# Kernel optimization log

Hardware: AMD Instinct MI355X
Metric: run time of the kernel (lower is better)

The kernel has to match this reference:

```python
import jax, jax.numpy as jnp
import numpy as np

CP_SIZE = 2
CP_RANK = 0
SLIDING_WINDOW = 1024
S_GLOBAL = 4096
T_LOCAL = S_GLOBAL // CP_SIZE
NQ, NK, HN = 16, 8, 128


def setup_inputs() -> dict:
    key = jax.random.key(0)
    kq, kk, kv = jax.random.split(key, 3)
    return {
        # local zigzag-sliced queries on this cp rank: [t_local, nq, hn]
        "query": jax.random.normal(kq, (T_LOCAL, NQ, HN), dtype=jnp.float32),
        # K/V AFTER all-gather across cp ranks (rank-chunk concatenated layout,
        # exactly what gather_from_sequence_parallel_region produces): [S, nk, hn]
        "key": jax.random.normal(kk, (S_GLOBAL, NK, HN), dtype=jnp.float32),
        "value": jax.random.normal(kv, (S_GLOBAL, NK, HN), dtype=jnp.float32),
        # global packed-seq boundaries (single sub-sequence)
        "cu_seqlens": jnp.array([0, S_GLOBAL], dtype=jnp.int32),
    }


def _zigzag_perm(seq_len_global: int, cp: int) -> jnp.ndarray:
    """global position g -> offset into the rank-gathered K/V tensor."""
    cs = seq_len_global // (2 * cp)
    g = jnp.arange(seq_len_global)
    q_idx = g // cs
    owner = jnp.where(q_idx < cp, q_idx, 2 * cp - 1 - q_idx)
    local_in_rank = jnp.where(q_idx < cp, g - owner * cs,
                              cs + (g - (2 * cp - 1 - owner) * cs))
    return owner * (2 * cs) + local_in_rank


def _zigzag_rows(local_len: int, rank: int, cp: int) -> jnp.ndarray:
    """global positions of this rank's local Q tokens (zigzag layout)."""
    cs = local_len // 2
    first = jnp.arange(rank * cs, (rank + 1) * cs)
    second = jnp.arange((2 * cp - rank - 1) * cs, (2 * cp - rank) * cs)
    return jnp.concatenate([first, second])


def reference(query, key, value, cu_seqlens):
    S = key.shape[0]
    t_local, nq, hn = query.shape
    nk = key.shape[1]
    scale = hn ** (-0.5)

    # un-permute gathered K/V from rank-chunk zigzag layout to global order
    perm = _zigzag_perm(S, CP_SIZE)
    k_full = key[perm]    # [S, nk, hn]
    v_full = value[perm]

    # GQA: replicate kv heads to match q heads (enable_gqa)
    rep = nq // nk
    k_full = jnp.repeat(k_full, rep, axis=1)  # [S, nq, hn]
    v_full = jnp.repeat(v_full, rep, axis=1)

    # causal + sliding-window mask from zigzag global row indices
    row = _zigzag_rows(t_local, CP_RANK, CP_SIZE)  # [t_local]
    col = jnp.arange(S)
    forbid = col[None, :] > row[:, None]
    if SLIDING_WINDOW is not None and SLIDING_WINDOW > 0:
        forbid = forbid | (col[None, :] < row[:, None] - (SLIDING_WINDOW - 1))
    bias = jnp.where(forbid, jnp.finfo(query.dtype).min, 0.0).astype(query.dtype)

    # SDPA: scores [nq, t_local, S]
    scores = jnp.einsum('shd,thd->hst', query, k_full) * scale + bias[None]
    probs = jax.nn.softmax(scores, axis=-1)
    out = jnp.einsum('hst,thd->shd', probs, v_full)  # [t_local, nq, hn]
    return out.reshape(t_local, nq * hn)
```

## Files before the change

### kernel.cpp

```cpp
#include <hip/hip_runtime.h>
#include <hip/hip_bf16.h>

#define T_LOCAL 2048
#define S_GLOBAL 4096
#define NQ 16
#define NK 8
#define HN 128

#define SCALE2 0.12753102541996022f

typedef __attribute__((ext_vector_type(8))) short short8;
typedef __attribute__((ext_vector_type(4))) float f32x4;

static __device__ __forceinline__ ushort f2bf(float x) {
  unsigned u = __builtin_bit_cast(unsigned, x);
  unsigned r = (u + 0x7fffu + ((u >> 16) & 1u)) >> 16;
  return (ushort)r;
}

static __device__ __forceinline__ void gload16(const ushort* g, ushort* lds) {
  __builtin_amdgcn_global_load_lds(
      (const __attribute__((address_space(1))) void*)g,
      (__attribute__((address_space(3))) void*)lds, 16, 0, 0);
}

__global__ void k_convert(const float* __restrict__ K, ushort* __restrict__ Kb) {
  size_t i = ((size_t)blockIdx.x * 256 + threadIdx.x) * 4;
  float4 v = *(const float4*)(K + i);
  ushort4 o;
  o.x = f2bf(v.x); o.y = f2bf(v.y); o.z = f2bf(v.z); o.w = f2bf(v.w);
  *(ushort4*)(Kb + i) = o;
}

__global__ void v_transpose(const float* __restrict__ V, ushort* __restrict__ Vt) {
  int bid = blockIdx.x;
  int h  = bid >> 7;
  int r  = bid & 127;
  int d0 = (r >> 6) << 6;
  int p0 = (r & 63) << 6;
  __shared__ ushort tile[64][72];
  int tx = threadIdx.x & 15, ty = threadIdx.x >> 4;
  #pragma unroll
  for (int it = 0; it < 4; ++it) {
    int p = p0 + it * 16 + ty;
    int d = tx * 4;
    float4 v = *(const float4*)(V + ((size_t)p * NK + h) * HN + d0 + d);
    tile[d + 0][it * 16 + ty] = f2bf(v.x);
    tile[d + 1][it * 16 + ty] = f2bf(v.y);
    tile[d + 2][it * 16 + ty] = f2bf(v.z);
    tile[d + 3][it * 16 + ty] = f2bf(v.w);
  }
  __syncthreads();
  #pragma unroll
  for (int it = 0; it < 4; ++it) {
    int d  = it * 16 + ty;
    int pb = tx * 4;
    ushort4 o;
    o.x = tile[d][pb + 0]; o.y = tile[d][pb + 1];
    o.z = tile[d][pb + 2]; o.w = tile[d][pb + 3];
    *(ushort4*)(Vt + ((size_t)h * HN + d0 + d) * S_GLOBAL + p0 + pb) = o;
  }
}

__global__ __launch_bounds__(512, 4)
void attn_kernel(const float* __restrict__ Q, const ushort* __restrict__ Kb,
                 const ushort* __restrict__ Vt, float* __restrict__ Out) {
  __shared__ ushort Klds[2][64 * 128];
  __shared__ ushort Vlds[2][128 * 64];
  __shared__ ushort Pl[8][16][56];

  const int lane = threadIdx.x & 63;
  const int w    = threadIdx.x >> 6;
  const int qg   = w & 3;
  const int ks   = w >> 2;
  const int qcol = lane & 15;
  const int g    = lane >> 4;

  const int bid  = blockIdx.x;
  const int kvh  = bid & 7;
  const int j    = bid >> 3;
  const int head = 2 * kvh + (j & 1);
  const int slot = j >> 1;
  const int Tt   = (slot & 1) ? 16 + (slot >> 1) : (slot >> 1);
  const int tb   = Tt << 6;
  const int tw   = tb + qg * 16;
  const int tq   = tw + qcol;

  int c0, nC, a0 = 0, n;
  if (tb < 1024) { c0 = 0; nC = Tt + 1; n = nC; }
  else { c0 = 16; nC = Tt - 15; a0 = Tt + 32; n = nC + (32 - Tt); }

  short8 qf[4];
  {
    const float* qb = Q + ((size_t)tq * NQ + head) * HN;
    #pragma unroll
    for (int ds = 0; ds < 4; ++ds) {
      const float4* p4 = (const float4*)(qb + ds * 32 + g * 8);
      float4 a = p4[0], b = p4[1];
      short8 f;
      f[0] = f2bf(a.x); f[1] = f2bf(a.y); f[2] = f2bf(a.z); f[3] = f2bf(a.w);
      f[4] = f2bf(b.x); f[5] = f2bf(b.y); f[6] = f2bf(b.z); f[7] = f2bf(b.w);
      qf[ds] = f;
    }
  }
  asm volatile("s_waitcnt vmcnt(0)" ::: "memory");

  f32x4 acc[8];
  #pragma unroll
  for (int i = 0; i < 8; ++i) acc[i] = (f32x4){0.f, 0.f, 0.f, 0.f};
  float m_run = -1e30f, l_run = 0.f;

  ushort* prow = &Pl[w][qcol][0];
  const int rx = (qcol & 7) << 4;

  auto chunk_p0 = [&](int i) {
    return ((i < nC) ? (c0 + i) : (a0 + (i - nC))) << 6;
  };

  auto stage = [&](int b, int p0) {
    #pragma unroll
    for (int t = 0; t < 2; ++t) {
      int idx = (w * 2 + t) * 64 + lane;
      int row = idx >> 4;
      int cu  = (idx & 15) ^ (row & 7);
      gload16(Kb + ((size_t)(p0 + row) * NK + kvh) * HN + cu * 8,
              &Klds[b][(w * 2 + t) * 512]);
    }
    #pragma unroll
    for (int t = 0; t < 2; ++t) {
      int idx = (w * 2 + t) * 64 + lane;
      int d   = idx >> 3;
      int pu  = (idx & 7) ^ (d & 7);
      gload16(Vt + ((size_t)kvh * HN + d) * S_GLOBAL + p0 + pu * 8,
              &Vlds[b][(w * 2 + t) * 512]);
    }
  };

  stage(0, chunk_p0(0));

  for (int c = 0; c < n; ++c) {
    if (c + 1 < n) {
      stage((c + 1) & 1, chunk_p0(c + 1));
      asm volatile("s_waitcnt vmcnt(4)" ::: "memory");
    } else {
      asm volatile("s_waitcnt vmcnt(0)" ::: "memory");
    }
    __builtin_amdgcn_s_barrier();

    const int p0   = chunk_p0(c);
    const bool anti = p0 >= 2048;
    const char* Klc = (const char*)Klds[c & 1];
    const char* Vlc = (const char*)Vlds[c & 1];

    const int p0s = p0 + ks * 32;
    const bool activ = anti ? (p0s + 31 >= tw + 2049) : (p0s <= tw + 15);
    if (activ) {
      const bool needmask = anti ? (p0s < tw + 2064) : (p0s + 31 > tw);

      short8 kf[2][4];
      #pragma unroll
      for (int sub = 0; sub < 2; ++sub) {
        const int rbase = (ks * 32 + sub * 16 + qcol) * 256;
        #pragma unroll
        for (int ds = 0; ds < 4; ++ds)
          kf[sub][ds] = *(const short8*)(Klc + rbase + ((ds * 64 + g * 16) ^ rx));
      }
      short8 vf[8];
      #pragma unroll
      for (int db = 0; db < 8; ++db)
        vf[db] = *(const short8*)(Vlc + (db * 16 + qcol) * 128 + ((ks * 64 + g * 16) ^ rx));

      f32x4 st[2];
      st[0] = (f32x4){0.f, 0.f, 0.f, 0.f};
      st[1] = (f32x4){0.f, 0.f, 0.f, 0.f};
      #pragma unroll
      for (int sub = 0; sub < 2; ++sub)
        #pragma unroll
        for (int ds = 0; ds < 4; ++ds)
          st[sub] = __builtin_amdgcn_mfma_f32_16x16x32_bf16(kf[sub][ds], qf[ds], st[sub], 0, 0, 0);

      float s_[8];
      #pragma unroll
      for (int sub = 0; sub < 2; ++sub) {
        #pragma unroll
        for (int r = 0; r < 4; ++r) {
          float sv = st[sub][r] * SCALE2;
          if (needmask) {
            int p = p0s + sub * 16 + g * 4 + r;
            bool ok = anti ? (p >= tq + 2049) : (p <= tq);
            sv = ok ? sv : -INFINITY;
          }
          s_[sub * 4 + r] = sv;
        }
      }

      float mt = s_[0];
      #pragma unroll
      for (int i = 1; i < 8; ++i) mt = fmaxf(mt, s_[i]);
      mt = fmaxf(mt, __shfl_xor(mt, 16));
      mt = fmaxf(mt, __shfl_xor(mt, 32));
      float mnew = fmaxf(m_run, mt);
      float fsc  = __builtin_amdgcn_exp2f(m_run - mnew);
      float pv[8];
      float ps = 0.f;
      #pragma unroll
      for (int i = 0; i < 8; ++i) { pv[i] = __builtin_amdgcn_exp2f(s_[i] - mnew); ps += pv[i]; }
      ps += __shfl_xor(ps, 16);
      ps += __shfl_xor(ps, 32);
      l_run = l_run * fsc + ps;
      m_run = mnew;
      #pragma unroll
      for (int i = 0; i < 8; ++i) acc[i] *= fsc;

      unsigned lo0 = (unsigned)f2bf(pv[0]) | ((unsigned)f2bf(pv[1]) << 16);
      unsigned hi0 = (unsigned)f2bf(pv[2]) | ((unsigned)f2bf(pv[3]) << 16);
      unsigned lo1 = (unsigned)f2bf(pv[4]) | ((unsigned)f2bf(pv[5]) << 16);
      unsigned hi1 = (unsigned)f2bf(pv[6]) | ((unsigned)f2bf(pv[7]) << 16);
      *(uint2*)(prow + g * 4)      = make_uint2(lo0, hi0);
      *(uint2*)(prow + 16 + g * 4) = make_uint2(lo1, hi1);
      short8 pf = *(const short8*)(prow + g * 8);

      #pragma unroll
      for (int db = 0; db < 8; ++db)
        acc[db] = __builtin_amdgcn_mfma_f32_16x16x32_bf16(vf[db], pf, acc[db], 0, 0, 0);
    }
    __builtin_amdgcn_s_barrier();
  }

  __syncthreads();
  float* mb  = (float*)&Klds[0][0];
  float* mlb = (float*)&Vlds[0][0];
  if (ks == 1) {
    if (g == 0) {
      mlb[(qg * 16 + qcol) * 2 + 0] = m_run;
      mlb[(qg * 16 + qcol) * 2 + 1] = l_run;
    }
    #pragma unroll
    for (int db = 0; db < 8; ++db)
      *(f32x4*)&mb[(qg * 16 + qcol) * 128 + db * 16 + g * 4] = acc[db];
  }
  __syncthreads();
  if (ks == 0) {
    float mr = mlb[(qg * 16 + qcol) * 2 + 0];
    float lr = mlb[(qg * 16 + qcol) * 2 + 1];
    float mnew = fmaxf(m_run, mr);
    float f0 = __builtin_amdgcn_exp2f(m_run - mnew);
    float fr = __builtin_amdgcn_exp2f(mr - mnew);
    float inv = 1.0f / (l_run * f0 + lr * fr);
    float* ob = Out + (size_t)tq * (NQ * HN) + head * HN + g * 4;
    #pragma unroll
    for (int db = 0; db < 8; ++db) {
      f32x4 o = *(const f32x4*)&mb[(qg * 16 + qcol) * 128 + db * 16 + g * 4];
      float4 r;
      r.x = (acc[db][0] * f0 + o[0] * fr) * inv;
      r.y = (acc[db][1] * f0 + o[1] * fr) * inv;
      r.z = (acc[db][2] * f0 + o[2] * fr) * inv;
      r.w = (acc[db][3] * f0 + o[3] * fr) * inv;
      *(float4*)(ob + db * 16) = r;
    }
  }
}

extern "C" void kernel_launch(void* const* d_in, const int* in_sizes, int n_in,
                              void* d_out, int out_size, void* d_ws, size_t ws_size,
                              hipStream_t stream) {
  const float* Q = (const float*)d_in[0];
  const float* K = (const float*)d_in[1];
  const float* V = (const float*)d_in[2];
  float* Out = (float*)d_out;

  ushort* Kb = (ushort*)d_ws;
  ushort* Vt = Kb + (size_t)S_GLOBAL * NK * HN;

  k_convert<<<dim3((S_GLOBAL * NK * HN) / (256 * 4)), dim3(256), 0, stream>>>(K, Kb);
  v_transpose<<<dim3(NK * 2 * (S_GLOBAL / 64)), dim3(256), 0, stream>>>(V, Vt);
  attn_kernel<<<dim3(512), dim3(512), 0, stream>>>(Q, Kb, Vt, Out);
}
```

Before: 140.2 us.

## Halve block query tile, drop LDS double buffer and P round-trip via permuted K rows

Each block now handles 32 query rows with 256 threads instead of 64 rows with 512, doubling the grid to 1024 blocks and halving LDS use per block so more blocks can be resident. The K/V double buffer is removed in favour of a single buffer that is loaded and waited on synchronously every chunk. K rows are read in a permuted order so the score MFMA output layout already matches the B-operand layout needed for the PV MFMA, which removes the P write/read through LDS. The cost is that load latency is no longer overlapped within a block, and each K/V chunk is fetched by twice as many blocks.

After: 166.6 us. +18.8%, slower.

```diff
diff --git a/kernel.cpp b/kernel.cpp
--- a/kernel.cpp
+++ b/kernel.cpp
@@ -62,17 +62,16 @@
   }
 }
 
-__global__ __launch_bounds__(512, 4)
+__global__ __launch_bounds__(256, 4)
 void attn_kernel(const float* __restrict__ Q, const ushort* __restrict__ Kb,
                  const ushort* __restrict__ Vt, float* __restrict__ Out) {
-  __shared__ ushort Klds[2][64 * 128];
-  __shared__ ushort Vlds[2][128 * 64];
-  __shared__ ushort Pl[8][16][56];
+  __shared__ ushort Klds[64 * 128];
+  __shared__ ushort Vlds[128 * 64];
 
   const int lane = threadIdx.x & 63;
   const int w    = threadIdx.x >> 6;
-  const int qg   = w & 3;
-  const int ks   = w >> 2;
+  const int qg   = w & 1;
+  const int ks   = w >> 1;
   const int qcol = lane & 15;
   const int g    = lane >> 4;
 
@@ -81,14 +80,17 @@
   const int j    = bid >> 3;
   const int head = 2 * kvh + (j & 1);
   const int slot = j >> 1;
-  const int Tt   = (slot & 1) ? 16 + (slot >> 1) : (slot >> 1);
-  const int tb   = Tt << 6;
+  const int Tt   = (slot & 1) ? 32 + (slot >> 1) : (slot >> 1);
+  const int tb   = Tt << 5;
   const int tw   = tb + qg * 16;
   const int tq   = tw + qcol;
 
   int c0, nC, a0 = 0, n;
-  if (tb < 1024) { c0 = 0; nC = Tt + 1; n = nC; }
-  else { c0 = 16; nC = Tt - 15; a0 = Tt + 32; n = nC + (32 - Tt); }
+  if (tb < 1024) { c0 = 0; nC = (tb >> 6) + 1; n = nC; }
+  else {
+    c0 = 16; nC = ((tb + 31) >> 6) - 15;
+    a0 = (tb + 2049) >> 6; n = nC + (64 - a0);
+  }
 
   short8 qf[4];
   {
@@ -103,54 +105,46 @@
       qf[ds] = f;
     }
   }
-  asm volatile("s_waitcnt vmcnt(0)" ::: "memory");
 
   f32x4 acc[8];
   #pragma unroll
   for (int i = 0; i < 8; ++i) acc[i] = (f32x4){0.f, 0.f, 0.f, 0.f};
   float m_run = -1e30f, l_run = 0.f;
 
-  ushort* prow = &Pl[w][qcol][0];
-  const int rx = (qcol & 7) << 4;
+  const int rxv = (qcol & 7) << 4;
 
   auto chunk_p0 = [&](int i) {
     return ((i < nC) ? (c0 + i) : (a0 + (i - nC))) << 6;
   };
 
-  auto stage = [&](int b, int p0) {
-    #pragma unroll
-    for (int t = 0; t < 2; ++t) {
-      int idx = (w * 2 + t) * 64 + lane;
+  auto stage = [&](int p0) {
+    #pragma unroll
+    for (int t = 0; t < 4; ++t) {
+      int idx = (w * 4 + t) * 64 + lane;
       int row = idx >> 4;
       int cu  = (idx & 15) ^ (row & 7);
       gload16(Kb + ((size_t)(p0 + row) * NK + kvh) * HN + cu * 8,
-              &Klds[b][(w * 2 + t) * 512]);
-    }
-    #pragma unroll
-    for (int t = 0; t < 2; ++t) {
-      int idx = (w * 2 + t) * 64 + lane;
+              &Klds[(w * 4 + t) * 512]);
+    }
+    #pragma unroll
+    for (int t = 0; t < 4; ++t) {
+      int idx = (w * 4 + t) * 64 + lane;
       int d   = idx >> 3;
       int pu  = (idx & 7) ^ (d & 7);
       gload16(Vt + ((size_t)kvh * HN + d) * S_GLOBAL + p0 + pu * 8,
-              &Vlds[b][(w * 2 + t) * 512]);
+              &Vlds[(w * 4 + t) * 512]);
     }
   };
 
-  stage(0, chunk_p0(0));
-
   for (int c = 0; c < n; ++c) {
-    if (c + 1 < n) {
-      stage((c + 1) & 1, chunk_p0(c + 1));
-      asm volatile("s_waitcnt vmcnt(4)" ::: "memory");
-    } else {
-      asm volatile("s_waitcnt vmcnt(0)" ::: "memory");
-    }
-    __builtin_amdgcn_s_barrier();
+    stage(chunk_p0(c));
+    asm volatile("s_waitcnt vmcnt(0)" ::: "memory");
+    __syncthreads();
 
     const int p0   = chunk_p0(c);
     const bool anti = p0 >= 2048;
-    const char* Klc = (const char*)Klds[c & 1];
-    const char* Vlc = (const char*)Vlds[c & 1];
+    const char* Klc = (const char*)Klds;
+    const char* Vlc = (const char*)Vlds;
 
     const int p0s = p0 + ks * 32;
     const bool activ = anti ? (p0s + 31 >= tw + 2049) : (p0s <= tw + 15);
@@ -160,15 +154,17 @@
       short8 kf[2][4];
       #pragma unroll
       for (int sub = 0; sub < 2; ++sub) {
-        const int rbase = (ks * 32 + sub * 16 + qcol) * 256;
+        const int krow = ks * 32 + ((qcol >> 2) << 3) + sub * 4 + (qcol & 3);
+        const int rbase = krow * 256;
+        const int rxk = (krow & 7) << 4;
         #pragma unroll
         for (int ds = 0; ds < 4; ++ds)
-          kf[sub][ds] = *(const short8*)(Klc + rbase + ((ds * 64 + g * 16) ^ rx));
+          kf[sub][ds] = *(const short8*)(Klc + rbase + ((ds * 64 + g * 16) ^ rxk));
       }
       short8 vf[8];
       #pragma unroll
       for (int db = 0; db < 8; ++db)
-        vf[db] = *(const short8*)(Vlc + (db * 16 + qcol) * 128 + ((ks * 64 + g * 16) ^ rx));
+        vf[db] = *(const short8*)(Vlc + (db * 16 + qcol) * 128 + ((ks * 64 + g * 16) ^ rxv));
 
       f32x4 st[2];
       st[0] = (f32x4){0.f, 0.f, 0.f, 0.f};
@@ -186,7 +182,7 @@
         for (int r = 0; r < 4; ++r) {
           float sv = st[sub][r] * SCALE2;
           if (needmask) {
-            int p = p0s + sub * 16 + g * 4 + r;
+            int p = p0s + g * 8 + sub * 4 + r;
             bool ok = anti ? (p >= tq + 2049) : (p <= tq);
             sv = ok ? sv : -INFINITY;
           }
@@ -212,24 +208,22 @@
       #pragma unroll
       for (int i = 0; i < 8; ++i) acc[i] *= fsc;
 
-      unsigned lo0 = (unsigned)f2bf(pv[0]) | ((unsigned)f2bf(pv[1]) << 16);
-      unsigned hi0 = (unsigned)f2bf(pv[2]) | ((unsigned)f2bf(pv[3]) << 16);
-      unsigned lo1 = (unsigned)f2bf(pv[4]) | ((unsigned)f2bf(pv[5]) << 16);
-      unsigned hi1 = (unsigned)f2bf(pv[6]) | ((unsigned)f2bf(pv[7]) << 16);
-      *(uint2*)(prow + g * 4)      = make_uint2(lo0, hi0);
-      *(uint2*)(prow + 16 + g * 4) = make_uint2(lo1, hi1);
-      short8 pf = *(const short8*)(prow + g * 8);
+      uint4 pu;
+      pu.x = (unsigned)f2bf(pv[0]) | ((unsigned)f2bf(pv[1]) << 16);
+      pu.y = (unsigned)f2bf(pv[2]) | ((unsigned)f2bf(pv[3]) << 16);
+      pu.z = (unsigned)f2bf(pv[4]) | ((unsigned)f2bf(pv[5]) << 16);
+      pu.w = (unsigned)f2bf(pv[6]) | ((unsigned)f2bf(pv[7]) << 16);
+      short8 pf = __builtin_bit_cast(short8, pu);
 
       #pragma unroll
       for (int db = 0; db < 8; ++db)
         acc[db] = __builtin_amdgcn_mfma_f32_16x16x32_bf16(vf[db], pf, acc[db], 0, 0, 0);
     }
-    __builtin_amdgcn_s_barrier();
-  }
-
-  __syncthreads();
-  float* mb  = (float*)&Klds[0][0];
-  float* mlb = (float*)&Vlds[0][0];
+    __syncthreads();
+  }
+
+  float* mb  = (float*)&Klds[0];
+  float* mlb = (float*)&Vlds[0];
   if (ks == 1) {
     if (g == 0) {
       mlb[(qg * 16 + qcol) * 2 + 0] = m_run;
@@ -274,5 +268,5 @@
 
   k_convert<<<dim3((S_GLOBAL * NK * HN) / (256 * 4)), dim3(256), 0, stream>>>(K, Kb);
   v_transpose<<<dim3(NK * 2 * (S_GLOBAL / 64)), dim3(256), 0, stream>>>(V, Vt);
-  attn_kernel<<<dim3(512), dim3(512), 0, stream>>>(Q, Kb, Vt, Out);
-}
+  attn_kernel<<<dim3(1024), dim3(256), 0, stream>>>(Q, Kb, Vt, Out);
+}
```
